# Kernel tuning notes

Hardware: AMD Instinct MI355X
Metric: run time of the kernel (lower is better)

## Reference

```python
import jax, jax.numpy as jnp
import numpy as np

EPS = 1e-5  # torch BatchNorm default eps


def _bn(x, gamma, beta, axes):
    # training-mode batch norm over `axes`, channel dim is axis 1
    mean = jnp.mean(x, axis=axes, keepdims=True)
    var = jnp.var(x, axis=axes, keepdims=True)
    shape = [1] * x.ndim
    shape[1] = -1
    return (x - mean) * jax.lax.rsqrt(var + EPS) * gamma.reshape(shape) + beta.reshape(shape)


def setup_inputs() -> dict:
    B, C, N = 16, 512, 192
    S_RATIO, R_RATIO = 4, 8
    Cs, Cr = C // S_RATIO, C // R_RATIO  # 128, 64
    inter = N * Cr + C  # 12800
    key = jax.random.key(0)
    ks = jax.random.split(key, 6)

    def w(k, shp, fan):
        return jax.random.normal(k, shp, jnp.float32) * np.float32(np.sqrt(2.0 / fan))

    return {
        "inputs": jax.random.normal(ks[0], (B, C, N), jnp.float32),
        "retain": 0,
        "theta_w": w(ks[1], (Cs, C), Cs), "theta_b": jnp.zeros((Cs,), jnp.float32),
        "theta_g": jnp.ones((Cs,), jnp.float32), "theta_be": jnp.zeros((Cs,), jnp.float32),
        "phi_w": w(ks[2], (Cs, C), Cs), "phi_b": jnp.zeros((Cs,), jnp.float32),
        "phi_g": jnp.ones((Cs,), jnp.float32), "phi_be": jnp.zeros((Cs,), jnp.float32),
        "re_w": w(ks[3], (Cr, Cs), Cr), "re_b": jnp.zeros((Cr,), jnp.float32),
        "re_g": jnp.ones((Cr,), jnp.float32), "re_be": jnp.zeros((Cr,), jnp.float32),
        "att_w": w(ks[4], (C, inter), C), "att_b": jnp.zeros((C,), jnp.float32),
        "att_g": jnp.ones((C,), jnp.float32), "att_be": jnp.zeros((C,), jnp.float32),
    }


def reference(inputs, retain, theta_w, theta_b, theta_g, theta_be,
              phi_w, phi_b, phi_g, phi_be, re_w, re_b, re_g, re_be,
              att_w, att_b, att_g, att_be):
    B, C, N = inputs.shape
    xt = inputs.transpose(0, 2, 1)  # [B, N, C]

    # theta / phi pro_blocks: Linear -> BN1d (over B,N) -> ReLU, output [B, Cs, N]
    th = jax.nn.relu(_bn(jnp.einsum('bnc,oc->bon', xt, theta_w) + theta_b[None, :, None], theta_g, theta_be, (0, 2)))
    ph = jax.nn.relu(_bn(jnp.einsum('bnc,oc->bon', xt, phi_w) + phi_b[None, :, None], phi_g, phi_be, (0, 2)))
    th = th.transpose(0, 2, 1)  # [B, N, Cs]
    ph = ph.transpose(0, 2, 1)  # [B, N, Cs]

    # pairwise broadcast-diff: [B, N, N, Cs]
    diff = th[:, :, None, :] - ph[:, None, :, :]

    # pro_block1: Linear -> BN2d -> ReLU, then flatten to [B, N, N*Cr]
    rel = jnp.einsum('bijc,oc->boij', diff, re_w) + re_b[None, :, None, None]  # [B, Cr, N, N]
    rel = jax.nn.relu(_bn(rel, re_g, re_be, (0, 2, 3)))
    rel = rel.transpose(0, 2, 3, 1).reshape(B, N, -1)  # [B, N, N*Cr]

    # attention_generator: Linear -> BN1d -> sigmoid, output [B, C, N]
    cat = jnp.concatenate([xt, rel], axis=2)  # [B, N, C + N*Cr]
    att = jnp.einsum('bni,oi->bon', cat, att_w) + att_b[None, :, None]  # [B, C, N]
    att = jax.nn.sigmoid(_bn(att, att_g, att_be, (0, 2)))

    features = att * inputs  # [B, C, N]
    if retain:
        return features
    return jnp.sum(features, axis=2) / jnp.sum(att, axis=2)  # [B, C]
```

## Files before the change

kernel.cpp:

```cpp
#include <hip/hip_runtime.h>

#define BB 16
#define CC 512
#define NN 192
#define CS 128
#define CR 64
#define EPSF 1e-5f
#define PART (BB*CC*NN)

typedef __attribute__((ext_vector_type(8))) short short8;
typedef __attribute__((ext_vector_type(4))) float f32x4;
typedef __attribute__((ext_vector_type(4))) unsigned int uint4v;

#define OFF_LIN2  0
#define OFF_P2    786432
#define OFF_QT    983040
#define OFF_ATTP4 1179648
#define OFF_WBF   7471104
#define OFF_XT    10747904
#define OFF_ROWS  11534336
#define OFF_SPART 11550720

__device__ __forceinline__ unsigned pkbf(float a, float b){
  unsigned r; asm("v_cvt_pk_bf16_f32 %0, %1, %2" : "=v"(r) : "v"(a), "v"(b)); return r;
}

__device__ __forceinline__ void gload_lds16(const void* g, void* l){
  __builtin_amdgcn_global_load_lds(
      (const __attribute__((address_space(1))) unsigned int*)g,
      (__attribute__((address_space(3))) unsigned int*)l, 16, 0, 0);
}

__global__ __launch_bounds__(256) void kconvxt(
    const float* __restrict__ aw, const float* __restrict__ x,
    short* __restrict__ wbf, short* __restrict__ xT)
{
  __shared__ float Ts[64][65];
  if (blockIdx.x < 3200) {
    int t = blockIdx.x*256 + threadIdx.x;
    int o2 = t / 1600;
    int kk = (t - o2*1600) * 8;
    const float* src = &aw[o2*12800 + kk];
    float4 v0 = *reinterpret_cast<const float4*>(src);
    float4 v1 = *reinterpret_cast<const float4*>(src+4);
    uint4v w;
    w.x = pkbf(v0.x, v0.y); w.y = pkbf(v0.z, v0.w);
    w.z = pkbf(v1.x, v1.y); w.w = pkbf(v1.z, v1.w);
    *reinterpret_cast<uint4v*>(&wbf[o2*12800 + kk]) = w;
  } else {
    int bid = blockIdx.x - 3200;
    int nt = bid % 3; int ct = (bid/3) & 7; int b = bid / 24;
    int c0 = ct*64, n0 = nt*64;
    int tid = threadIdx.x;
    int col = tid & 63, r0 = tid >> 6;
    #pragma unroll
    for (int it = 0; it < 16; ++it){
      int r = r0 + it*4;
      Ts[r][col] = x[(b*CC + c0 + r)*NN + n0 + col];
    }
    __syncthreads();
    #pragma unroll
    for (int it = 0; it < 2; ++it){
      int cp = it*256 + tid;
      int nr = cp >> 3, cc8 = (cp & 7)*8;
      uint4v wv;
      wv.x = pkbf(Ts[cc8+0][nr], Ts[cc8+1][nr]);
      wv.y = pkbf(Ts[cc8+2][nr], Ts[cc8+3][nr]);
      wv.z = pkbf(Ts[cc8+4][nr], Ts[cc8+5][nr]);
      wv.w = pkbf(Ts[cc8+6][nr], Ts[cc8+7][nr]);
      *reinterpret_cast<uint4v*>(&xT[((b*NN) + n0 + nr)*CC + c0 + cc8]) = wv;
    }
  }
}

__global__ __launch_bounds__(256) void k1_lin(
    const float* __restrict__ x, const float* __restrict__ wth,
    const float* __restrict__ wph, float* __restrict__ lin2,
    float* __restrict__ spart)
{
  int bid = blockIdx.x;
  int nt = bid % 3; int ch = (bid/3) & 1; int b = (bid/6) & 15; int path = bid/96;
  int cs0 = ch*64, n0 = nt*64;
  const float* w = path ? wph : wth;
  int tid = threadIdx.x;
  int ty = tid >> 4, tx = tid & 15;
  __shared__ float Xs[32][64];
  __shared__ float Ws[32][68];
  float acc[4][4];
  #pragma unroll
  for (int i=0;i<4;++i)
    #pragma unroll
    for (int j=0;j<4;++j) acc[i][j]=0.f;
  for (int c0 = 0; c0 < CC; c0 += 32){
    __syncthreads();
    {
      int nn = tid & 63, cb = tid >> 6;
      #pragma unroll
      for (int it = 0; it < 8; ++it)
        Xs[cb + it*4][nn] = x[(b*CC + c0 + cb + it*4)*NN + n0 + nn];
    }
    {
      int cc = tid & 31, sb = tid >> 5;
      #pragma unroll
      for (int it = 0; it < 8; ++it)
        Ws[cc][sb + it*8] = w[(cs0 + sb + it*8)*CC + c0 + cc];
    }
    __syncthreads();
    #pragma unroll 8
    for (int cc = 0; cc < 32; ++cc){
      float w4[4], x4[4];
      *reinterpret_cast<float4*>(w4) = *reinterpret_cast<const float4*>(&Ws[cc][ty*4]);
      *reinterpret_cast<float4*>(x4) = *reinterpret_cast<const float4*>(&Xs[cc][tx*4]);
      #pragma unroll
      for (int i=0;i<4;++i)
        #pragma unroll
        for (int j=0;j<4;++j) acc[i][j] += w4[i]*x4[j];
    }
  }
  #pragma unroll
  for (int r = 0; r < 4; ++r){
    int cs = cs0 + ty*4 + r;
    float4 v = make_float4(acc[r][0],acc[r][1],acc[r][2],acc[r][3]);
    *reinterpret_cast<float4*>(&lin2[(b*256 + path*128 + cs)*NN + n0 + tx*4]) = v;
  }
  #pragma unroll
  for (int r = 0; r < 4; ++r){
    float s = acc[r][0]+acc[r][1]+acc[r][2]+acc[r][3];
    float q = acc[r][0]*acc[r][0]+acc[r][1]*acc[r][1]
            + acc[r][2]*acc[r][2]+acc[r][3]*acc[r][3];
    #pragma unroll
    for (int off=8; off; off>>=1){ s += __shfl_down(s,off,16); q += __shfl_down(q,off,16); }
    if (tx==0){
      int cs2 = path*128 + cs0 + ty*4 + r;
      spart[cs2*48 + b*3 + nt] = s;
      spart[12288 + cs2*48 + b*3 + nt] = q;
    }
  }
}

__global__ __launch_bounds__(256) void k3_gemm(
    const float* __restrict__ lin2, const float* __restrict__ spart,
    const float* __restrict__ tg, const float* __restrict__ tbe,
    const float* __restrict__ pg, const float* __restrict__ pbe,
    const float* __restrict__ rw,
    float* __restrict__ p2raw, float* __restrict__ qTraw,
    float* __restrict__ rows4)
{
  int bid = blockIdx.x;
  int ih = bid & 3; int b = (bid>>2) & 15; int path = bid >> 6;
  int i0 = ih*48;
  __shared__ float Ls[128][48];
  __shared__ float Ws[64][132];
  __shared__ float sscl[512];
  int tid = threadIdx.x;
  {
    int c2 = tid;
    float s=0.f, q=0.f;
    #pragma unroll 8
    for (int i=0;i<48;++i){ s += spart[c2*48+i]; q += spart[12288+c2*48+i]; }
    float mean = s * (1.f/3072.f);
    float var = q * (1.f/3072.f) - mean*mean;
    int pth = c2 >> 7, c = c2 & 127;
    float g  = pth ? pg[c]  : tg[c];
    float be = pth ? pbe[c] : tbe[c];
    float a = g * rsqrtf(var + EPSF);
    sscl[c2] = a; sscl[256+c2] = be - mean*a;
  }
  __syncthreads();
  #pragma unroll
  for (int it = 0; it < 6; ++it){
    int cp = it*256 + tid;
    int row = cp / 12, c4 = cp - row*12;
    float a = sscl[path*128 + row], d = sscl[256 + path*128 + row];
    float4 v = *reinterpret_cast<const float4*>(&lin2[(b*256 + path*128 + row)*NN + i0 + c4*4]);
    float4 r;
    r.x = fmaxf(a*v.x + d, 0.f); r.y = fmaxf(a*v.y + d, 0.f);
    r.z = fmaxf(a*v.z + d, 0.f); r.w = fmaxf(a*v.w + d, 0.f);
    *reinterpret_cast<float4*>(&Ls[row][c4*4]) = r;
  }
  #pragma unroll
  for (int it = 0; it < 8; ++it){
    int cp = it*256 + tid;
    int o = cp >> 5, c4 = cp & 31;
    *reinterpret_cast<float4*>(&Ws[o][c4*4]) =
      *reinterpret_cast<const float4*>(&rw[o*CS + c4*4]);
  }
  __syncthreads();
  int oy = tid >> 4, ix = tid & 15;
  float acc[4][3];
  #pragma unroll
  for (int r=0;r<4;++r)
    #pragma unroll
    for (int e=0;e<3;++e) acc[r][e]=0.f;
  #pragma unroll 4
  for (int c = 0; c < 128; ++c){
    float w4[4], l3[3];
    #pragma unroll
    for (int r=0;r<4;++r) w4[r] = Ws[oy*4+r][c];
    #pragma unroll
    for (int e=0;e<3;++e) l3[e] = Ls[c][ix*3+e];
    #pragma unroll
    for (int r=0;r<4;++r)
      #pragma unroll
      for (int e=0;e<3;++e) acc[r][e] += w4[r]*l3[e];
  }
  float* dst = path ? qTraw : p2raw;
  #pragma unroll
  for (int r=0;r<4;++r)
    #pragma unroll
    for (int e=0;e<3;++e)
      dst[(b*NN + i0 + ix*3 + e)*64 + oy*4 + r] = acc[r][e];
  #pragma unroll
  for (int r=0;r<4;++r){
    float s = acc[r][0]+acc[r][1]+acc[r][2];
    float q = acc[r][0]*acc[r][0]+acc[r][1]*acc[r][1]+acc[r][2]*acc[r][2];
    #pragma unroll
    for (int off=8; off; off>>=1){ s += __shfl_down(s,off,16); q += __shfl_down(q,off,16); }
    if (ix==0){
      int o = oy*4+r;
      int ri = (path*1024 + b*64 + o)*4 + ih;
      rows4[ri] = s; rows4[8192 + ri] = q;
    }
  }
}

__global__ __launch_bounds__(256) void k5_mfma(
    const short* __restrict__ wbf, const short* __restrict__ xT,
    const float* __restrict__ p2raw, const float* __restrict__ qTraw,
    const float* __restrict__ rows4,
    const float* __restrict__ rg, const float* __restrict__ rbe,
    float* __restrict__ attp4)
{
  int bid = blockIdx.x;
  int nt = bid & 1, mt = (bid >> 1) & 3, b = (bid >> 3) & 15, ks = bid >> 7;
  int o20 = mt*128, n0 = nt*96;
  int j0 = ks*48;

  int tid = threadIdx.x;
  int w = tid >> 6, lane = tid & 63;
  int wr = w >> 1, wc = w & 1;
  int l15 = lane & 15, l4 = lane >> 4;
  int cq = tid & 7;

  __shared__ __align__(16) short As[128*64];
  __shared__ __align__(16) short Bs[96*64];
  __shared__ __align__(16) float qlds[2][64];
  __shared__ float srel[128];

  if (tid < 64){
    int o = tid;
    float sa=0,saq=0,sb=0,sbq=0,cross=0;
    for (int bb=0;bb<BB;++bb){
      float ra=0, rb=0;
      #pragma unroll
      for (int ih=0; ih<4; ++ih){
        int ia = (bb*64+o)*4 + ih, ib = (1024 + bb*64+o)*4 + ih;
        ra += rows4[ia]; rb += rows4[ib];
        saq += rows4[8192 + ia]; sbq += rows4[8192 + ib];
      }
      sa += ra; sb += rb; cross += ra*rb;
    }
    float mean = (sa - sb) * (1.f/3072.f);
    float e2 = (saq + sbq) * (1.f/3072.f) - cross * (2.f/589824.f);
    float var = e2 - mean*mean;
    float s = rg[o] * rsqrtf(var + EPSF);
    srel[o] = s;
    srel[64+o] = rbe[o] - s*mean;
  }
  __syncthreads();

  float pr[3][8];
  {
    float sc8[8], sh8[8];
    #pragma unroll
    for (int k=0;k<8;++k){ sc8[k] = srel[cq*8+k]; sh8[k] = srel[64+cq*8+k]; }
    #pragma unroll
    for (int it=0; it<3; ++it){
      int n = it*32 + (tid >> 3);
      const float* pp = &p2raw[(size_t)((b*NN) + n0 + n)*64 + cq*8];
      float4 u0 = *reinterpret_cast<const float4*>(pp);
      float4 u1 = *reinterpret_cast<const float4*>(pp+4);
      pr[it][0]=sc8[0]*u0.x+sh8[0]; pr[it][1]=sc8[1]*u0.y+sh8[1];
      pr[it][2]=sc8[2]*u0.z+sh8[2]; pr[it][3]=sc8[3]*u0.w+sh8[3];
      pr[it][4]=sc8[4]*u1.x+sh8[4]; pr[it][5]=sc8[5]*u1.y+sh8[5];
      pr[it][6]=sc8[6]*u1.z+sh8[6]; pr[it][7]=sc8[7]*u1.w+sh8[7];
    }
  }
  if (tid < 64) qlds[0][tid] = srel[tid] * qTraw[(size_t)(b*NN + j0)*64 + tid];

  auto stageA = [&](int colbase){
    #pragma unroll
    for (int it=0; it<4; ++it){
      int cp = w*256 + it*64 + lane;
      int row = cp >> 3, c = (cp & 7) ^ (row & 7);
      gload_lds16(&wbf[(o20 + row)*12800 + colbase + c*8],
                  &As[(w*256 + it*64)*8]);
    }
  };
  auto stageBx = [&](int colbase){
    #pragma unroll
    for (int it=0; it<3; ++it){
      int cp = w*192 + it*64 + lane;
      int row = cp >> 3, c = (cp & 7) ^ (row & 7);
      gload_lds16(&xT[(size_t)((b*NN) + n0 + row)*CC + colbase + c*8],
                  &Bs[(w*192 + it*64)*8]);
    }
  };

  f32x4 acc[4][3];
  #pragma unroll
  for (int mi=0;mi<4;++mi)
    #pragma unroll
    for (int ni=0;ni<3;++ni) acc[mi][ni] = (f32x4){0.f,0.f,0.f,0.f};

  auto mfma_phase = [&](){
    __builtin_amdgcn_s_setprio(1);
    #pragma unroll
    for (int s=0; s<2; ++s){
      short8 av[4], bv[3];
      int c = s*4 + l4;
      #pragma unroll
      for (int mi=0; mi<4; ++mi){
        int row = wr*64 + mi*16 + l15;
        av[mi] = *reinterpret_cast<const short8*>(&As[row*64 + ((c ^ (row&7))<<3)]);
      }
      #pragma unroll
      for (int ni=0; ni<3; ++ni){
        int rown = wc*48 + ni*16 + l15;
        bv[ni] = *reinterpret_cast<const short8*>(&Bs[rown*64 + ((c ^ (rown&7))<<3)]);
      }
      #pragma unroll
      for (int mi=0; mi<4; ++mi)
        #pragma unroll
        for (int ni=0; ni<3; ++ni)
          acc[mi][ni] = __builtin_amdgcn_mfma_f32_16x16x32_bf16(av[mi], bv[ni], acc[mi][ni], 0, 0, 0);
    }
    __builtin_amdgcn_s_setprio(0);
  };

  #pragma unroll
  for (int kt = 0; kt < 2; ++kt){
    __syncthreads();
    stageA(ks*128 + kt*64);
    stageBx(ks*128 + kt*64);
    __syncthreads();
    mfma_phase();
  }

  for (int kt = 0; kt < 48; ++kt){
    __syncthreads();
    stageA(512 + (j0 + kt)*64);
    if (tid < 64 && kt < 47)
      qlds[(kt+1)&1][tid] = srel[tid] * qTraw[(size_t)(b*NN + j0 + kt + 1)*64 + tid];
    {
      const float* qq = qlds[kt&1];
      float4 qa = *reinterpret_cast<const float4*>(&qq[cq*8]);
      float4 qb = *reinterpret_cast<const float4*>(&qq[cq*8+4]);
      #pragma unroll
      for (int it=0; it<3; ++it){
        float r0 = fmaxf(pr[it][0]-qa.x, 0.f);
        float r1 = fmaxf(pr[it][1]-qa.y, 0.f);
        float r2 = fmaxf(pr[it][2]-qa.z, 0.f);
        float r3 = fmaxf(pr[it][3]-qa.w, 0.f);
        float r4 = fmaxf(pr[it][4]-qb.x, 0.f);
        float r5 = fmaxf(pr[it][5]-qb.y, 0.f);
        float r6 = fmaxf(pr[it][6]-qb.z, 0.f);
        float r7 = fmaxf(pr[it][7]-qb.w, 0.f);
        uint4v wv;
        wv.x = pkbf(r0,r1); wv.y = pkbf(r2,r3);
        wv.z = pkbf(r4,r5); wv.w = pkbf(r6,r7);
        int n = it*32 + (tid >> 3);
        *reinterpret_cast<uint4v*>(&Bs[n*64 + ((cq ^ (n&7))<<3)]) = wv;
      }
    }
    __syncthreads();
    mfma_phase();
  }

  float* dst = attp4 + (size_t)ks*PART;
  #pragma unroll
  for (int mi=0; mi<4; ++mi){
    #pragma unroll
    for (int r=0; r<4; ++r){
      int o2 = o20 + wr*64 + mi*16 + l4*4 + r;
      #pragma unroll
      for (int ni=0; ni<3; ++ni){
        int n = n0 + wc*48 + ni*16 + l15;
        dst[(b*CC + o2)*NN + n] = acc[mi][ni][r];
      }
    }
  }
}

__global__ __launch_bounds__(256) void k67(
    const float* __restrict__ p4, const float* __restrict__ x,
    const float* __restrict__ g, const float* __restrict__ be,
    float* __restrict__ out)
{
  int o2 = blockIdx.x;
  int tid = threadIdx.x;
  int b = tid >> 4, nl = tid & 15;
  int base = (b*CC + o2)*NN + nl;
  float v[12], xv[12];
  float s=0.f, q=0.f;
  #pragma unroll
  for (int it=0; it<12; ++it){
    int idx = base + it*16;
    float t = p4[idx] + p4[PART+idx] + p4[2*PART+idx] + p4[3*PART+idx];
    v[it] = t; s += t; q += t*t;
    xv[it] = x[idx];
  }
  __shared__ float rs[4], rq[4], ad[2];
  #pragma unroll
  for (int off=32; off; off>>=1){ s += __shfl_down(s,off); q += __shfl_down(q,off); }
  int w = tid >> 6;
  if ((tid & 63)==0){ rs[w]=s; rq[w]=q; }
  __syncthreads();
  if (tid==0){
    s = rs[0]+rs[1]+rs[2]+rs[3]; q = rq[0]+rq[1]+rq[2]+rq[3];
    float mean = s * (1.f/3072.f);
    float var = q * (1.f/3072.f) - mean*mean;
    float a = g[o2] * rsqrtf(var + EPSF);
    ad[0] = a; ad[1] = be[o2] - mean*a;
  }
  __syncthreads();
  float a = ad[0], d = ad[1];
  float sf=0.f, ss=0.f;
  #pragma unroll
  for (int it=0; it<12; ++it){
    float sig = 1.f/(1.f + expf(-(a*v[it] + d)));
    sf += sig * xv[it]; ss += sig;
  }
  #pragma unroll
  for (int off=8; off; off>>=1){ sf += __shfl_down(sf,off,16); ss += __shfl_down(ss,off,16); }
  if (nl==0) out[b*CC + o2] = sf/ss;
}

extern "C" void kernel_launch(void* const* d_in, const int* in_sizes, int n_in,
                              void* d_out, int out_size, void* d_ws, size_t ws_size,
                              hipStream_t stream)
{
  const float* inputs  = (const float*)d_in[0];
  const float* theta_w = (const float*)d_in[2];
  const float* theta_g = (const float*)d_in[4];
  const float* theta_be= (const float*)d_in[5];
  const float* phi_w   = (const float*)d_in[6];
  const float* phi_g   = (const float*)d_in[8];
  const float* phi_be  = (const float*)d_in[9];
  const float* re_w    = (const float*)d_in[10];
  const float* re_g    = (const float*)d_in[12];
  const float* re_be   = (const float*)d_in[13];
  const float* att_w   = (const float*)d_in[14];
  const float* att_g   = (const float*)d_in[16];
  const float* att_be  = (const float*)d_in[17];

  float* ws = (float*)d_ws;
  float* lin2  = ws + OFF_LIN2;
  float* p2raw = ws + OFF_P2;
  float* qTraw = ws + OFF_QT;
  float* attp4 = ws + OFF_ATTP4;
  short* wbf   = (short*)(ws + OFF_WBF);
  short* xT    = (short*)(ws + OFF_XT);
  float* rows4 = ws + OFF_ROWS;
  float* spart = ws + OFF_SPART;

  kconvxt<<<3584, 256, 0, stream>>>(att_w, inputs, wbf, xT);
  k1_lin<<<192, 256, 0, stream>>>(inputs, theta_w, phi_w, lin2, spart);
  k3_gemm<<<128, 256, 0, stream>>>(lin2, spart, theta_g, theta_be, phi_g, phi_be,
                                   re_w, p2raw, qTraw, rows4);
  k5_mfma<<<512, 256, 0, stream>>>(wbf, xT, p2raw, qTraw, rows4, re_g, re_be, attp4);
  k67<<<512, 256, 0, stream>>>(attp4, inputs, att_g, att_be, (float*)d_out);
}
```

Measured before the change: 132.5 us.

## Split small GEMM kernels into more blocks and parallelize BN stat reduction

Doubles the grid of k1_lin (32 output channels per block) and k3_gemm (24 columns per block) so these small launches fill more of the 256 CUs. The per-row partial stats grow from 4 to 8 slices, and k5_mfma now reduces them with all 256 threads through shared memory instead of 64. It also drops the s_setprio hints around the MFMA phase and vectorizes the k67 loads to float2. The cost is less data reuse per block and more partial-sum traffic.

```diff
diff --git a/kernel.cpp b/kernel.cpp
--- a/kernel.cpp
+++ b/kernel.cpp
@@ -19,7 +19,7 @@
 #define OFF_WBF   7471104
 #define OFF_XT    10747904
 #define OFF_ROWS  11534336
-#define OFF_SPART 11550720
+#define OFF_SPART 11567104
 
 __device__ __forceinline__ unsigned pkbf(float a, float b){
   unsigned r; asm("v_cvt_pk_bf16_f32 %0, %1, %2" : "=v"(r) : "v"(a), "v"(b)); return r;
@@ -79,16 +79,16 @@
     float* __restrict__ spart)
 {
   int bid = blockIdx.x;
-  int nt = bid % 3; int ch = (bid/3) & 1; int b = (bid/6) & 15; int path = bid/96;
-  int cs0 = ch*64, n0 = nt*64;
+  int nt = bid % 3; int ch = (bid/3) & 3; int b = (bid/12) & 15; int path = bid/192;
+  int cs0 = ch*32, n0 = nt*64;
   const float* w = path ? wph : wth;
   int tid = threadIdx.x;
   int ty = tid >> 4, tx = tid & 15;
   __shared__ float Xs[32][64];
-  __shared__ float Ws[32][68];
-  float acc[4][4];
-  #pragma unroll
-  for (int i=0;i<4;++i)
+  __shared__ float Ws[32][36];
+  float acc[2][4];
+  #pragma unroll
+  for (int i=0;i<2;++i)
     #pragma unroll
     for (int j=0;j<4;++j) acc[i][j]=0.f;
   for (int c0 = 0; c0 < CC; c0 += 32){
@@ -102,36 +102,36 @@
     {
       int cc = tid & 31, sb = tid >> 5;
       #pragma unroll
-      for (int it = 0; it < 8; ++it)
+      for (int it = 0; it < 4; ++it)
         Ws[cc][sb + it*8] = w[(cs0 + sb + it*8)*CC + c0 + cc];
     }
     __syncthreads();
     #pragma unroll 8
     for (int cc = 0; cc < 32; ++cc){
-      float w4[4], x4[4];
-      *reinterpret_cast<float4*>(w4) = *reinterpret_cast<const float4*>(&Ws[cc][ty*4]);
+      float w2[2], x4[4];
+      w2[0] = Ws[cc][ty*2]; w2[1] = Ws[cc][ty*2+1];
       *reinterpret_cast<float4*>(x4) = *reinterpret_cast<const float4*>(&Xs[cc][tx*4]);
       #pragma unroll
-      for (int i=0;i<4;++i)
+      for (int i=0;i<2;++i)
         #pragma unroll
-        for (int j=0;j<4;++j) acc[i][j] += w4[i]*x4[j];
-    }
-  }
-  #pragma unroll
-  for (int r = 0; r < 4; ++r){
-    int cs = cs0 + ty*4 + r;
+        for (int j=0;j<4;++j) acc[i][j] += w2[i]*x4[j];
+    }
+  }
+  #pragma unroll
+  for (int r = 0; r < 2; ++r){
+    int cs = cs0 + ty*2 + r;
     float4 v = make_float4(acc[r][0],acc[r][1],acc[r][2],acc[r][3]);
     *reinterpret_cast<float4*>(&lin2[(b*256 + path*128 + cs)*NN + n0 + tx*4]) = v;
   }
   #pragma unroll
-  for (int r = 0; r < 4; ++r){
+  for (int r = 0; r < 2; ++r){
     float s = acc[r][0]+acc[r][1]+acc[r][2]+acc[r][3];
     float q = acc[r][0]*acc[r][0]+acc[r][1]*acc[r][1]
             + acc[r][2]*acc[r][2]+acc[r][3]*acc[r][3];
     #pragma unroll
     for (int off=8; off; off>>=1){ s += __shfl_down(s,off,16); q += __shfl_down(q,off,16); }
     if (tx==0){
-      int cs2 = path*128 + cs0 + ty*4 + r;
+      int cs2 = path*128 + cs0 + ty*2 + r;
       spart[cs2*48 + b*3 + nt] = s;
       spart[12288 + cs2*48 + b*3 + nt] = q;
     }
@@ -144,12 +144,12 @@
     const float* __restrict__ pg, const float* __restrict__ pbe,
     const float* __restrict__ rw,
     float* __restrict__ p2raw, float* __restrict__ qTraw,
-    float* __restrict__ rows4)
+    float* __restrict__ rows8)
 {
   int bid = blockIdx.x;
-  int ih = bid & 3; int b = (bid>>2) & 15; int path = bid >> 6;
-  int i0 = ih*48;
-  __shared__ float Ls[128][48];
+  int ih = bid & 7; int b = (bid>>3) & 15; int path = bid >> 7;
+  int i0 = ih*24;
+  __shared__ float Ls[128][24];
   __shared__ float Ws[64][132];
   __shared__ float sscl[512];
   int tid = threadIdx.x;
@@ -168,9 +168,9 @@
   }
   __syncthreads();
   #pragma unroll
-  for (int it = 0; it < 6; ++it){
+  for (int it = 0; it < 3; ++it){
     int cp = it*256 + tid;
-    int row = cp / 12, c4 = cp - row*12;
+    int row = cp / 6, c4 = cp - row*6;
     float a = sscl[path*128 + row], d = sscl[256 + path*128 + row];
     float4 v = *reinterpret_cast<const float4*>(&lin2[(b*256 + path*128 + row)*NN + i0 + c4*4]);
     float4 r;
@@ -186,40 +186,40 @@
       *reinterpret_cast<const float4*>(&rw[o*CS + c4*4]);
   }
   __syncthreads();
-  int oy = tid >> 4, ix = tid & 15;
-  float acc[4][3];
-  #pragma unroll
-  for (int r=0;r<4;++r)
+  int oy = tid >> 3, ix = tid & 7;
+  float acc[2][3];
+  #pragma unroll
+  for (int r=0;r<2;++r)
     #pragma unroll
     for (int e=0;e<3;++e) acc[r][e]=0.f;
   #pragma unroll 4
   for (int c = 0; c < 128; ++c){
-    float w4[4], l3[3];
-    #pragma unroll
-    for (int r=0;r<4;++r) w4[r] = Ws[oy*4+r][c];
+    float w2[2], l3[3];
+    #pragma unroll
+    for (int r=0;r<2;++r) w2[r] = Ws[oy*2+r][c];
     #pragma unroll
     for (int e=0;e<3;++e) l3[e] = Ls[c][ix*3+e];
     #pragma unroll
-    for (int r=0;r<4;++r)
-      #pragma unroll
-      for (int e=0;e<3;++e) acc[r][e] += w4[r]*l3[e];
+    for (int r=0;r<2;++r)
+      #pragma unroll
+      for (int e=0;e<3;++e) acc[r][e] += w2[r]*l3[e];
   }
   float* dst = path ? qTraw : p2raw;
   #pragma unroll
-  for (int r=0;r<4;++r)
+  for (int r=0;r<2;++r)
     #pragma unroll
     for (int e=0;e<3;++e)
-      dst[(b*NN + i0 + ix*3 + e)*64 + oy*4 + r] = acc[r][e];
-  #pragma unroll
-  for (int r=0;r<4;++r){
+      dst[(b*NN + i0 + ix*3 + e)*64 + oy*2 + r] = acc[r][e];
+  #pragma unroll
+  for (int r=0;r<2;++r){
     float s = acc[r][0]+acc[r][1]+acc[r][2];
     float q = acc[r][0]*acc[r][0]+acc[r][1]*acc[r][1]+acc[r][2]*acc[r][2];
     #pragma unroll
-    for (int off=8; off; off>>=1){ s += __shfl_down(s,off,16); q += __shfl_down(q,off,16); }
+    for (int off=4; off; off>>=1){ s += __shfl_down(s,off,8); q += __shfl_down(q,off,8); }
     if (ix==0){
-      int o = oy*4+r;
-      int ri = (path*1024 + b*64 + o)*4 + ih;
-      rows4[ri] = s; rows4[8192 + ri] = q;
+      int o = oy*2+r;
+      int ri = (path*1024 + b*64 + o)*8 + ih;
+      rows8[ri] = s; rows8[16384 + ri] = q;
     }
   }
 }
@@ -227,7 +227,7 @@
 __global__ __launch_bounds__(256) void k5_mfma(
     const short* __restrict__ wbf, const short* __restrict__ xT,
     const float* __restrict__ p2raw, const float* __restrict__ qTraw,
-    const float* __restrict__ rows4,
+    const float* __restrict__ rows8,
     const float* __restrict__ rg, const float* __restrict__ rbe,
     float* __restrict__ attp4)
 {
@@ -246,19 +246,33 @@
   __shared__ __align__(16) short Bs[96*64];
   __shared__ __align__(16) float qlds[2][64];
   __shared__ float srel[128];
-
+  __shared__ float sred[4][5][64];
+
+  {
+    int o = tid & 63, g = tid >> 6;
+    float sa=0,sb=0,saq=0,sbq=0,cross=0;
+    #pragma unroll
+    for (int bb=g*4; bb<g*4+4; ++bb){
+      float ra=0, rb=0;
+      #pragma unroll
+      for (int ih=0; ih<8; ++ih){
+        int ia = (bb*64+o)*8 + ih, ib = (1024 + bb*64+o)*8 + ih;
+        ra += rows8[ia]; rb += rows8[ib];
+        saq += rows8[16384 + ia]; sbq += rows8[16384 + ib];
+      }
+      sa += ra; sb += rb; cross += ra*rb;
+    }
+    sred[g][0][o]=sa; sred[g][1][o]=sb; sred[g][2][o]=saq;
+    sred[g][3][o]=sbq; sred[g][4][o]=cross;
+  }
+  __syncthreads();
   if (tid < 64){
     int o = tid;
-    float sa=0,saq=0,sb=0,sbq=0,cross=0;
-    for (int bb=0;bb<BB;++bb){
-      float ra=0, rb=0;
-      #pragma unroll
-      for (int ih=0; ih<4; ++ih){
-        int ia = (bb*64+o)*4 + ih, ib = (1024 + bb*64+o)*4 + ih;
-        ra += rows4[ia]; rb += rows4[ib];
-        saq += rows4[8192 + ia]; sbq += rows4[8192 + ib];
-      }
-      sa += ra; sb += rb; cross += ra*rb;
+    float sa=0,sb=0,saq=0,sbq=0,cross=0;
+    #pragma unroll
+    for (int g=0; g<4; ++g){
+      sa += sred[g][0][o]; sb += sred[g][1][o]; saq += sred[g][2][o];
+      sbq += sred[g][3][o]; cross += sred[g][4][o];
     }
     float mean = (sa - sb) * (1.f/3072.f);
     float e2 = (saq + sbq) * (1.f/3072.f) - cross * (2.f/589824.f);
@@ -314,7 +328,6 @@
     for (int ni=0;ni<3;++ni) acc[mi][ni] = (f32x4){0.f,0.f,0.f,0.f};
 
   auto mfma_phase = [&](){
-    __builtin_amdgcn_s_setprio(1);
     #pragma unroll
     for (int s=0; s<2; ++s){
       short8 av[4], bv[3];
@@ -335,7 +348,6 @@
         for (int ni=0; ni<3; ++ni)
           acc[mi][ni] = __builtin_amdgcn_mfma_f32_16x16x32_bf16(av[mi], bv[ni], acc[mi][ni], 0, 0, 0);
     }
-    __builtin_amdgcn_s_setprio(0);
   };
 
   #pragma unroll
@@ -400,15 +412,22 @@
   int o2 = blockIdx.x;
   int tid = threadIdx.x;
   int b = tid >> 4, nl = tid & 15;
-  int base = (b*CC + o2)*NN + nl;
   float v[12], xv[12];
   float s=0.f, q=0.f;
   #pragma unroll
-  for (int it=0; it<12; ++it){
-    int idx = base + it*16;
-    float t = p4[idx] + p4[PART+idx] + p4[2*PART+idx] + p4[3*PART+idx];
-    v[it] = t; s += t; q += t*t;
-    xv[it] = x[idx];
+  for (int it=0; it<6; ++it){
+    int n = nl*2 + it*32;
+    int idx = (b*CC + o2)*NN + n;
+    float t0=0.f, t1=0.f;
+    #pragma unroll
+    for (int p=0; p<4; ++p){
+      float2 u = *reinterpret_cast<const float2*>(&p4[(size_t)p*PART + idx]);
+      t0 += u.x; t1 += u.y;
+    }
+    float2 xu = *reinterpret_cast<const float2*>(&x[idx]);
+    v[it*2] = t0; v[it*2+1] = t1;
+    xv[it*2] = xu.x; xv[it*2+1] = xu.y;
+    s += t0 + t1; q += t0*t0 + t1*t1;
   }
   __shared__ float rs[4], rq[4], ad[2];
   #pragma unroll
@@ -461,13 +480,13 @@
   float* attp4 = ws + OFF_ATTP4;
   short* wbf   = (short*)(ws + OFF_WBF);
   short* xT    = (short*)(ws + OFF_XT);
-  float* rows4 = ws + OFF_ROWS;
+  float* rows8 = ws + OFF_ROWS;
   float* spart = ws + OFF_SPART;
 
   kconvxt<<<3584, 256, 0, stream>>>(att_w, inputs, wbf, xT);
-  k1_lin<<<192, 256, 0, stream>>>(inputs, theta_w, phi_w, lin2, spart);
-  k3_gemm<<<128, 256, 0, stream>>>(lin2, spart, theta_g, theta_be, phi_g, phi_be,
-                                   re_w, p2raw, qTraw, rows4);
-  k5_mfma<<<512, 256, 0, stream>>>(wbf, xT, p2raw, qTraw, rows4, re_g, re_be, attp4);
+  k1_lin<<<384, 256, 0, stream>>>(inputs, theta_w, phi_w, lin2, spart);
+  k3_gemm<<<256, 256, 0, stream>>>(lin2, spart, theta_g, theta_be, phi_g, phi_be,
+                                   re_w, p2raw, qTraw, rows8);
+  k5_mfma<<<512, 256, 0, stream>>>(wbf, xT, p2raw, qTraw, rows8, re_g, re_be, attp4);
   k67<<<512, 256, 0, stream>>>(attp4, inputs, att_g, att_be, (float*)d_out);
 }
```

Result: faster. 128.4 us (-3.1%).
